# Optimization experiments

Hardware: AMD Instinct MI355X
Metric: run time of the kernel (lower is better)

## Reference

```python
import jax, jax.numpy as jnp
import numpy as np

B, C, D, H = 128, 8, 1024, 8
K_RANGE = (2, 3, 4, 5)


def setup_inputs() -> dict:
    key = jax.random.key(0)
    ks = jax.random.split(key, 10)
    s = 0.02
    return {
        "x": jax.random.normal(ks[0], (B, D), jnp.float32),
        # per-K prototype groups, shape (nb_classes, K, embed_dim) as in get_prototype_group()
        "p2": jax.random.normal(ks[1], (C, 2, D), jnp.float32),
        "p3": jax.random.normal(ks[2], (C, 3, D), jnp.float32),
        "p4": jax.random.normal(ks[3], (C, 4, D), jnp.float32),
        "p5": jax.random.normal(ks[4], (C, 5, D), jnp.float32),
        # per-class attention Block params (stacked over class axis)
        "ln_g": jnp.ones((C, D), jnp.float32),
        "ln_b": jnp.zeros((C, D), jnp.float32),
        "w_qkv": jax.random.normal(ks[5], (C, 3 * D, D), jnp.float32) * s,
        "b_qkv": jnp.zeros((C, 3 * D), jnp.float32),
        "w_proj": jax.random.normal(ks[6], (C, D, D), jnp.float32) * s,
        "b_proj": jnp.zeros((C, D), jnp.float32),
        # cls head
        "w_cls": jax.random.normal(ks[7], (C, D), jnp.float32) * s,
        "b_cls": jnp.zeros((C,), jnp.float32),
    }


def _proto_group(x, pg):
    """x: (B,D); pg: (C,K,D). Returns nearest proto (B,D), per-sample class group (B,K,D), class ids (B,)."""
    Cc, K, d = pg.shape
    flat = pg.reshape(Cc * K, d)
    # squared L2 distances (argmin identical to torch.cdist p=2 argmin)
    d2 = (jnp.sum(x * x, axis=1, keepdims=True)
          - 2.0 * (x @ flat.T)
          + jnp.sum(flat * flat, axis=1))
    idx = jnp.argmin(d2, axis=1)          # (B,)
    cls = idx // K                        # (B,)
    return flat[idx], pg[cls], cls


def _vicreg(x, nearest, proto_space, sim_c=25.0, std_c=25.0, cov_c=1.0):
    # sim: pull x toward its nearest prototype in every K-group
    repr_loss = jnp.mean((x[:, None, :] - nearest) ** 2)
    # std over batch of prototype space, unbiased var, eps=1e-4
    std = jnp.sqrt(jnp.var(proto_space, axis=0, ddof=1) + 1e-4)   # (S,D)
    std_loss = jnp.mean(jax.nn.relu(1.0 - std))
    # covariance of centered flattened prototype space
    ps = proto_space - jnp.mean(proto_space, axis=0)
    P = ps.reshape(-1, ps.shape[-1])                              # (B*S, D)
    cov = P.T @ P / (P.shape[0] - 1)
    cov_loss = ((cov ** 2).sum() - (jnp.diagonal(cov) ** 2).sum()) / ps.shape[-1]
    return sim_c * repr_loss + std_c * std_loss + cov_c * cov_loss


def _forward(x, p2, p3, p4, p5, ln_g, ln_b, w_qkv, b_qkv, w_proj, b_proj, w_cls, b_cls):
    groups = (p2, p3, p4, p5)
    nearest_list, space_list, cls = [], [], None
    for pg in groups:
        n, sp, cls = _proto_group(x, pg)   # cls kept from LAST group, as in torch code
        nearest_list.append(n)
        space_list.append(sp)
    nearest = jnp.stack(nearest_list, axis=1)     # (B, len(K_range), D)
    proto_space = jnp.concatenate(space_list, 1)  # (B, sum(K_range), D)

    vcr = _vicreg(x, nearest, proto_space)

    # per-class attention Block: LayerNorm -> MHA -> residual, vectorized over class axis c
    S = proto_space.shape[1]
    mu = proto_space.mean(-1, keepdims=True)
    var = proto_space.var(-1, keepdims=True)
    xn = (proto_space - mu) * jax.lax.rsqrt(var + 1e-5)               # (B,S,D)
    h = xn[None] * ln_g[:, None, None, :] + ln_b[:, None, None, :]    # (C,B,S,D)

    qkv = jnp.einsum('cbsd,cfd->cbsf', h, w_qkv) + b_qkv[:, None, None, :]
    dh = D // H
    qkv = qkv.reshape(C, B, S, 3, H, dh).transpose(3, 0, 1, 4, 2, 5)  # (3,C,B,H,S,dh)
    q, k, v = qkv[0] * (dh ** -0.5), qkv[1], qkv[2]
    attn = jax.nn.softmax(jnp.einsum('cbhqe,cbhke->cbhqk', q, k), axis=-1)
    o = jnp.einsum('cbhqk,cbhke->cbhqe', attn, v)                     # (C,B,H,S,dh)
    o = o.transpose(0, 1, 3, 2, 4).reshape(C, B, S, D)
    out = jnp.einsum('cbsd,ced->cbse', o, w_proj) + b_proj[:, None, None, :]
    attended = proto_space[None] + out                                # (C,B,S,D)

    # route each sample through the block of its (last-group) assigned class
    cond = attended[cls, jnp.arange(B)]                               # (B,S,D)
    cond = cond / jnp.maximum(jnp.linalg.norm(cond, axis=2, keepdims=True), 1e-12)
    pooled = cond.mean(1)                                             # (B,D)
    logits = pooled @ w_cls.T + b_cls
    return logits, vcr


def reference(x, p2, p3, p4, p5, ln_g, ln_b, w_qkv, b_qkv, w_proj, b_proj, w_cls, b_cls):
    return _forward(x, p2, p3, p4, p5, ln_g, ln_b, w_qkv, b_qkv, w_proj, b_proj, w_cls, b_cls)
```

## Files before the change

### kernel.cpp

```cpp
#include <hip/hip_runtime.h>
#include <math.h>

#define NB 128
#define ND 1024
#define NS 14
#define NDH 128

typedef float f32x4 __attribute__((ext_vector_type(4)));
typedef short bf16x8 __attribute__((ext_vector_type(8)));
typedef unsigned int u32x4 __attribute__((ext_vector_type(4)));

__device__ __forceinline__ unsigned short f2bf(float v) {
  unsigned int u = __builtin_bit_cast(unsigned int, v);
  return (unsigned short)((u + 0x7FFFu + ((u >> 16) & 1u)) >> 16);
}
__device__ __forceinline__ float bf2f(unsigned short u) {
  return __builtin_bit_cast(float, (unsigned int)u << 16);
}

__device__ __forceinline__ bf16x8 pack_bv(float4 w0, float4 w1) {
  unsigned int u0, u1, u2, u3;
  asm("v_cvt_pk_bf16_f32 %0, %1, %2" : "=v"(u0) : "v"(w0.x), "v"(w0.y));
  asm("v_cvt_pk_bf16_f32 %0, %1, %2" : "=v"(u1) : "v"(w0.z), "v"(w0.w));
  asm("v_cvt_pk_bf16_f32 %0, %1, %2" : "=v"(u2) : "v"(w1.x), "v"(w1.y));
  asm("v_cvt_pk_bf16_f32 %0, %1, %2" : "=v"(u3) : "v"(w1.z), "v"(w1.w));
  u32x4 u = {u0, u1, u2, u3};
  return __builtin_bit_cast(bf16x8, u);
}

__device__ __forceinline__ void s_decomp(int s, int& g, int& k) {
  if (s < 2)      { g = 0; k = s; }
  else if (s < 5) { g = 1; k = s - 2; }
  else if (s < 9) { g = 2; k = s - 5; }
  else            { g = 3; k = s - 9; }
}
__device__ __forceinline__ const float* grp_ptr(int g, const float* p2, const float* p3,
                                                const float* p4, const float* p5) {
  return g == 0 ? p2 : g == 1 ? p3 : g == 2 ? p4 : p5;
}
__device__ __forceinline__ int grp_base(int g) { return g == 0 ? 0 : g == 1 ? 16 : g == 2 ? 40 : 72; }
__device__ __forceinline__ int grp_k(int g) { return g + 2; }

__global__ __launch_bounds__(256) void k_ln(
    const float* __restrict__ p2, const float* __restrict__ p3,
    const float* __restrict__ p4, const float* __restrict__ p5,
    const float* __restrict__ ln_g, const float* __restrict__ ln_b,
    unsigned short* __restrict__ hbf2, float* __restrict__ pall)
{
  int r = blockIdx.x, t = threadIdx.x;
  __shared__ __align__(16) float xs[ND];
  float4* xs4 = (float4*)xs;
  const float* pp; int idx;
  if (r < 16)      { pp = p2; idx = r; }
  else if (r < 40) { pp = p3; idx = r - 16; }
  else if (r < 72) { pp = p4; idx = r - 40; }
  else             { pp = p5; idx = r - 72; }
  const float4* row4 = (const float4*)(pp + (size_t)idx * ND);
  float4 v = row4[t];
  xs4[t] = v;
  float s1 = v.x + v.y + v.z + v.w;
  float s2 = v.x * v.x + v.y * v.y + v.z * v.z + v.w * v.w;
  __shared__ float ra[256], rb[256];
  ra[t] = s1; rb[t] = s2; __syncthreads();
  for (int o = 128; o > 0; o >>= 1) { if (t < o) { ra[t] += ra[t + o]; rb[t] += rb[t + o]; } __syncthreads(); }
  __shared__ float mu, rstd;
  if (t == 0) {
    float m = ra[0] * (1.f / 1024.f);
    float var = rb[0] * (1.f / 1024.f) - m * m;
    mu = m; rstd = rsqrtf(var + 1e-5f);
  }
  __syncthreads();
  ((float4*)(pall + (size_t)r * ND))[t] = xs4[t];
  float4 xv = xs4[t];
  float nx = (xv.x - mu) * rstd, ny = (xv.y - mu) * rstd,
        nz = (xv.z - mu) * rstd, nw = (xv.w - mu) * rstd;
  int d0 = t * 4;
  int m = r >> 4, rr = r & 15;
  int kblk = d0 >> 5, qq = (d0 >> 3) & 3, e0 = d0 & 7;
  size_t fidx = (size_t)kblk * 3584 + m * 512 + (qq * 16 + rr) * 8 + e0;
#pragma unroll
  for (int c = 0; c < 8; ++c) {
    float4 g = ((const float4*)(ln_g + (size_t)c * ND))[t];
    float4 bb = ((const float4*)(ln_b + (size_t)c * ND))[t];
    ushort4 u;
    u.x = f2bf(nx * g.x + bb.x); u.y = f2bf(ny * g.y + bb.y);
    u.z = f2bf(nz * g.z + bb.z); u.w = f2bf(nw * g.w + bb.w);
    *(ushort4*)&hbf2[(size_t)c * 114688 + fidx] = u;
  }
}

__global__ __launch_bounds__(512) void k_qkv_assign(
    const unsigned short* __restrict__ hbf2, const float* __restrict__ w_qkv,
    const float* __restrict__ b_qkv, unsigned short* __restrict__ qkv_bf,
    const float* __restrict__ x,
    const float* __restrict__ p2, const float* __restrict__ p3,
    const float* __restrict__ p4, const float* __restrict__ p5,
    int* __restrict__ cls, int* __restrict__ rows_g, float* __restrict__ minv)
{
  __shared__ __align__(16) float lred[3 * 2 * 7 * 256];
  int bid = blockIdx.x, t = threadIdx.x;
  if (bid < 768) {
    int c = bid / 96, xb = bid - c * 96;
    int lane = t & 63, wid = t >> 6;
    int cg = wid & 1, ks = wid >> 1;
    int r16 = lane & 15, q = lane >> 4;
    int col = xb * 32 + cg * 16 + r16;
    const float* Wp = w_qkv + ((size_t)c * 3072 + col) * ND + ks * 256 + q * 8;
    const unsigned short* Hp = hbf2 + (size_t)c * 114688 + (size_t)(ks * 8) * 3584 + lane * 8;
    f32x4 acc[7] = {};
#pragma unroll
    for (int i = 0; i < 8; ++i) {
      float4 w0 = *(const float4*)(Wp + i * 32);
      float4 w1 = *(const float4*)(Wp + i * 32 + 4);
      bf16x8 bv = pack_bv(w0, w1);
      const unsigned short* hk = Hp + (size_t)i * 3584;
#pragma unroll
      for (int m = 0; m < 7; ++m) {
        bf16x8 av = *(const bf16x8*)(hk + m * 512);
        acc[m] = __builtin_amdgcn_mfma_f32_16x16x32_bf16(av, bv, acc[m], 0, 0, 0);
      }
    }
    if (ks) {
#pragma unroll
      for (int m = 0; m < 7; ++m)
        *(f32x4*)&lred[(((ks - 1) * 2 + cg) * 7 + m) * 256 + lane * 4] = acc[m];
    }
    __syncthreads();
    if (ks == 0) {
      float bq = b_qkv[(size_t)c * 3072 + col];
#pragma unroll
      for (int m = 0; m < 7; ++m) {
        f32x4 a1 = *(const f32x4*)&lred[((0 * 2 + cg) * 7 + m) * 256 + lane * 4];
        f32x4 a2 = *(const f32x4*)&lred[((1 * 2 + cg) * 7 + m) * 256 + lane * 4];
        f32x4 a3 = *(const f32x4*)&lred[((2 * 2 + cg) * 7 + m) * 256 + lane * 4];
#pragma unroll
        for (int r = 0; r < 4; ++r) {
          int row = m * 16 + q * 4 + r;
          qkv_bf[((size_t)c * 112 + row) * 3072 + col] = f2bf(acc[m][r] + a1[r] + a2[r] + a3[r] + bq);
        }
      }
    }
  } else {
    int b = bid - 768;
    float4* xs4 = (float4*)lred;
    float* d2s = lred + 1024;
    int* cls_s = (int*)(lred + 1152);
    if (t < 256) {
      const float4* xg4 = (const float4*)(x + (size_t)b * ND);
      xs4[t] = xg4[t];
    }
    __syncthreads();
    if (t < 112) {
      const float* pp; int idx;
      if (t < 16)      { pp = p2; idx = t; }
      else if (t < 40) { pp = p3; idx = t - 16; }
      else if (t < 72) { pp = p4; idx = t - 40; }
      else             { pp = p5; idx = t - 72; }
      const float4* pr4 = (const float4*)(pp + (size_t)idx * ND);
      float acc = 0.f;
#pragma unroll 8
      for (int d = 0; d < 256; ++d) {
        float4 a = xs4[d], p = pr4[d];
        float dx = a.x - p.x, dy = a.y - p.y, dz = a.z - p.z, dw = a.w - p.w;
        acc += dx * dx + dy * dy + dz * dz + dw * dw;
      }
      d2s[t] = acc;
    }
    __syncthreads();
    if (t < 4) {
      int base = grp_base(t), kg = grp_k(t), cnt = 8 * kg;
      float mv = d2s[base]; int mi = 0;
      for (int j = 1; j < cnt; ++j) { float v = d2s[base + j]; if (v < mv) { mv = v; mi = j; } }
      int c = mi / kg;
      cls[b * 4 + t] = c; cls_s[t] = c;
      minv[b * 4 + t] = mv;
    }
    __syncthreads();
    if (t < NS) {
      int g, k; s_decomp(t, g, k);
      rows_g[b * NS + t] = grp_base(g) + cls_s[g] * grp_k(g) + k;
    }
  }
}

__global__ __launch_bounds__(128) void k_prep(
    const int* __restrict__ cls, const float* __restrict__ minv,
    int* __restrict__ counts, int* __restrict__ ccnt, int* __restrict__ order,
    int* __restrict__ posof, int* __restrict__ chunkidx, int* __restrict__ chunk_c,
    int* __restrict__ chunk_lo, int* __restrict__ chunkN, float* __restrict__ scal)
{
  __shared__ int cnt_s[32];
  __shared__ int cc_s[8];
  __shared__ float red[128];
  int t = threadIdx.x;
  if (t < 32) cnt_s[t] = 0;
  if (t < 8) cc_s[t] = 0;
  if (t < 4) scal[t] = 0.f;
  __syncthreads();
  int c3;
#pragma unroll
  for (int g = 0; g < 4; ++g) {
    int c = cls[t * 4 + g];
    atomicAdd(&cnt_s[g * 8 + c], 1);
    if (g == 3) c3 = c;
  }
  int pos = atomicAdd(&cc_s[c3], 1);
  order[c3 * 128 + pos] = t;
  posof[t] = pos;
  red[t] = minv[t * 4 + 0] + minv[t * 4 + 1] + minv[t * 4 + 2] + minv[t * 4 + 3];
  __syncthreads();
  for (int o = 64; o > 0; o >>= 1) { if (t < o) red[t] += red[t + o]; __syncthreads(); }
  if (t == 0) {
    scal[0] = red[0];
    int T = 0;
    for (int c = 0; c < 8; ++c) {
      chunkidx[c] = T;
      int nch = (cc_s[c] + 15) >> 4;
      for (int j = 0; j < nch; ++j) { chunk_c[T] = c; chunk_lo[T] = j * 16; ++T; }
    }
    chunkN[0] = T;
  }
  if (t < 32) counts[t] = cnt_s[t];
  if (t < 8) ccnt[t] = cc_s[t];
}

__global__ __launch_bounds__(256) void k_attn_stats(
    const unsigned short* __restrict__ qkv_bf, const int* __restrict__ cls,
    const int* __restrict__ rows_g, const int* __restrict__ posof,
    const int* __restrict__ chunkidx, unsigned short* __restrict__ obf2,
    const float* __restrict__ p2, const float* __restrict__ p3,
    const float* __restrict__ p4, const float* __restrict__ p5,
    const int* __restrict__ counts, float* __restrict__ M, float* __restrict__ scal)
{
  int bid = blockIdx.x, t = threadIdx.x;
  if (bid < 1024) {
    __shared__ __align__(16) float qs[NS * NDH], ks2[NS * NDH], vs[NS * NDH];
    __shared__ float sc[NS * NS];
    __shared__ int rg[NS];
    int h = bid & 7, b = bid >> 3;
    if (t < NS) rg[t] = rows_g[b * NS + t];
    __syncthreads();
    int cp = cls[b * 4 + 3];
    int pos = posof[b];
    size_t gbase = (size_t)(chunkidx[cp] + (pos >> 4)) * 229376;
    int slot = pos & 15;
    const float scale = 0.08838834764831843f;
    for (int i = t; i < NS * 32; i += 256) {
      int s = i >> 5, e4 = (i & 31) * 4;
      size_t base = ((size_t)cp * 112 + rg[s]) * 3072 + h * NDH + e4;
      ushort4 uq = *(const ushort4*)&qkv_bf[base];
      ushort4 uk = *(const ushort4*)&qkv_bf[base + 1024];
      ushort4 uv = *(const ushort4*)&qkv_bf[base + 2048];
      int o = s * NDH + e4;
      qs[o]     = bf2f(uq.x) * scale; qs[o + 1] = bf2f(uq.y) * scale;
      qs[o + 2] = bf2f(uq.z) * scale; qs[o + 3] = bf2f(uq.w) * scale;
      ks2[o]     = bf2f(uk.x); ks2[o + 1] = bf2f(uk.y);
      ks2[o + 2] = bf2f(uk.z); ks2[o + 3] = bf2f(uk.w);
      vs[o]     = bf2f(uv.x); vs[o + 1] = bf2f(uv.y);
      vs[o + 2] = bf2f(uv.z); vs[o + 3] = bf2f(uv.w);
    }
    __syncthreads();
    if (t < NS * NS) {
      int si = t / NS, sj = t - (t / NS) * NS;
      const float4* qa = (const float4*)&qs[si * NDH];
      const float4* kb = (const float4*)&ks2[sj * NDH];
      float acc = 0.f;
#pragma unroll 8
      for (int e4 = 0; e4 < 32; ++e4) {
        float4 a = qa[e4], k4 = kb[e4];
        acc += a.x * k4.x + a.y * k4.y + a.z * k4.z + a.w * k4.w;
      }
      sc[t] = acc;
    }
    __syncthreads();
    if (t < NS) {
      float mx = -1e30f;
      for (int j = 0; j < NS; ++j) mx = fmaxf(mx, sc[t * NS + j]);
      float e_[NS]; float sum = 0.f;
      for (int j = 0; j < NS; ++j) { float e = expf(sc[t * NS + j] - mx); e_[j] = e; sum += e; }
      float inv = 1.f / sum;
      for (int j = 0; j < NS; ++j) sc[t * NS + j] = e_[j] * inv;
    }
    __syncthreads();
    for (int i = t; i < NS * 32; i += 256) {
      int s = i >> 5, e4 = i & 31;
      float4 a = {0.f, 0.f, 0.f, 0.f};
#pragma unroll
      for (int j = 0; j < NS; ++j) {
        float w = sc[s * NS + j];
        float4 v4 = ((const float4*)&vs[j * NDH])[e4];
        a.x += w * v4.x; a.y += w * v4.y; a.z += w * v4.z; a.w += w * v4.w;
      }
      int row = slot * 14 + s;
      int m = row >> 4, r16 = row & 15;
      int d0 = h * NDH + e4 * 4;
      int kblk = d0 >> 5, qq = (d0 >> 3) & 3, e0 = d0 & 7;
      ushort4 u; u.x = f2bf(a.x); u.y = f2bf(a.y); u.z = f2bf(a.z); u.w = f2bf(a.w);
      *(ushort4*)&obf2[gbase + (size_t)kblk * 7168 + m * 512 + (qq * 16 + r16) * 8 + e0] = u;
    }
  } else {
    int idx = (bid - 1024) * 256 + t;
    int s = idx >> 10, d = idx & 1023;
    int g, k; s_decomp(s, g, k);
    const float* pp = grp_ptr(g, p2, p3, p4, p5);
    int kg = grp_k(g);
    float vc[8], nc[8];
    float sum = 0.f, sumsq = 0.f;
#pragma unroll
    for (int c = 0; c < 8; ++c) {
      float v = pp[((size_t)(c * kg + k)) * ND + d];
      float n = (float)counts[g * 8 + c];
      vc[c] = v; nc[c] = n;
      sum += n * v; sumsq += n * v * v;
    }
    float mean = sum * (1.f / 128.f);
    float var = (sumsq - 128.f * mean * mean) * (1.f / 127.f);
    float sd = sqrtf(var + 1e-4f);
#pragma unroll
    for (int c = 0; c < 8; ++c)
      M[((size_t)(s * 8 + c)) * ND + d] = sqrtf(nc[c] * (1.f / 1791.f)) * (vc[c] - mean);
    float part = fmaxf(1.f - sd, 0.f);
    __shared__ float red[256];
    red[t] = part; __syncthreads();
    for (int o = 128; o > 0; o >>= 1) { if (t < o) red[t] += red[t + o]; __syncthreads(); }
    if (t == 0) atomicAdd(&scal[1], red[0]);
  }
}

__global__ __launch_bounds__(512) void k_proj_gram(
    const unsigned short* __restrict__ obf2, const int* __restrict__ order,
    const int* __restrict__ ccnt, const int* __restrict__ chunk_c,
    const int* __restrict__ chunk_lo, const int* __restrict__ chunkN,
    const int* __restrict__ rows_g,
    const float* __restrict__ w_proj, const float* __restrict__ b_proj,
    const float* __restrict__ pall, float* __restrict__ att,
    const float* __restrict__ M, float* __restrict__ scal)
{
  int bid = blockIdx.x, t = threadIdx.x;
  if (bid < 960) {
    int g = bid / 64, xb = bid - g * 64;
    if (g >= chunkN[0]) return;
    __shared__ __align__(16) float lred[3 * 2 * 7 * 256];
    __shared__ int sid_s[16];
    int c = chunk_c[g], lo = chunk_lo[g];
    int cnt = ccnt[c];
    int nb = cnt - lo; if (nb > 16) nb = 16;
    int lane = t & 63, wid = t >> 6;
    int rh = wid & 1, ks = wid >> 1;
    if (t < 16) sid_s[t] = order[c * 128 + lo + ((t < nb) ? t : nb - 1)];
    int r16 = lane & 15, q = lane >> 4;
    int col = xb * 16 + r16;
    const float* Wp = w_proj + ((size_t)c * ND + col) * ND + ks * 256 + q * 8;
    const unsigned short* Ap = obf2 + (size_t)g * 229376 + (size_t)(ks * 8) * 7168 + rh * 3584 + lane * 8;
    f32x4 acc[7] = {};
#pragma unroll
    for (int i = 0; i < 8; ++i) {
      float4 w0 = *(const float4*)(Wp + i * 32);
      float4 w1 = *(const float4*)(Wp + i * 32 + 4);
      bf16x8 bv = pack_bv(w0, w1);
      const unsigned short* ak = Ap + (size_t)i * 7168;
#pragma unroll
      for (int m = 0; m < 7; ++m) {
        bf16x8 av = *(const bf16x8*)(ak + m * 512);
        acc[m] = __builtin_amdgcn_mfma_f32_16x16x32_bf16(av, bv, acc[m], 0, 0, 0);
      }
    }
    if (ks) {
#pragma unroll
      for (int m = 0; m < 7; ++m)
        *(f32x4*)&lred[(((ks - 1) * 2 + rh) * 7 + m) * 256 + lane * 4] = acc[m];
    }
    __syncthreads();
    if (ks == 0) {
      float bp = b_proj[(size_t)c * ND + col];
#pragma unroll
      for (int m = 0; m < 7; ++m) {
        f32x4 a1 = *(const f32x4*)&lred[((0 * 2 + rh) * 7 + m) * 256 + lane * 4];
        f32x4 a2 = *(const f32x4*)&lred[((1 * 2 + rh) * 7 + m) * 256 + lane * 4];
        f32x4 a3 = *(const f32x4*)&lred[((2 * 2 + rh) * 7 + m) * 256 + lane * 4];
#pragma unroll
        for (int r = 0; r < 4; ++r) {
          int row = rh * 112 + m * 16 + q * 4 + r;
          int slot = row / 14, s = row - slot * 14;
          if (slot < nb) {
            int b = sid_s[slot];
            float res = pall[(size_t)rows_g[b * NS + s] * ND + col];
            att[((size_t)b * NS + s) * ND + col] = acc[m][r] + a1[r] + a2[r] + a3[r] + bp + res;
          }
        }
      }
    }
  } else if (bid < 1072) {
    int r = bid - 960;
    __shared__ __align__(16) float mi[ND];
    __shared__ float red2[128];
    float4* mi4 = (float4*)mi;
    const float4* src4 = (const float4*)(M + (size_t)r * ND);
    if (t < 256) mi4[t] = src4[t];
    if (t < 128) red2[t] = 0.f;
    __syncthreads();
    int j = t >> 2, qd = t & 3;
    float p = 0.f;
    if (j < 112) {
      const float4* mj4 = (const float4*)(M + (size_t)j * ND);
      float acc = 0.f;
#pragma unroll 8
      for (int d = qd * 64; d < qd * 64 + 64; ++d) {
        float4 a = mi4[d], b = mj4[d];
        acc += a.x * b.x + a.y * b.y + a.z * b.z + a.w * b.w;
      }
      acc += __shfl_xor(acc, 1, 4);
      acc += __shfl_xor(acc, 2, 4);
      p = acc * acc;
    }
    if (qd == 0 && j < 112) red2[j] = p;
    __syncthreads();
    for (int o = 64; o > 0; o >>= 1) { if (t < o) red2[t] += red2[t + o]; __syncthreads(); }
    if (t == 0) atomicAdd(&scal[2], red2[0]);
  } else {
    int d = (bid - 1072) * 512 + t;
    float tsum = 0.f;
    for (int r = 0; r < 112; ++r) { float v = M[(size_t)r * ND + d]; tsum += v * v; }
    __shared__ float red3[512];
    red3[t] = tsum * tsum; __syncthreads();
    for (int o = 256; o > 0; o >>= 1) { if (t < o) red3[t] += red3[t + o]; __syncthreads(); }
    if (t == 0) atomicAdd(&scal[3], red3[0]);
  }
}

__global__ __launch_bounds__(256) void k_final(
    const float* __restrict__ att, const float* __restrict__ w_cls,
    const float* __restrict__ b_cls, const float* __restrict__ scal,
    float* __restrict__ out)
{
  int b = blockIdx.x, t = threadIdx.x;
  __shared__ __align__(16) float as[NS * ND];
  __shared__ float wred[NS][4];
  __shared__ float inv[NS];
  __shared__ __align__(16) float pooled[ND];
  int lane = t & 63, w = t >> 6;
#pragma unroll
  for (int s = 0; s < NS; ++s) {
    float4 v = ((const float4*)(att + ((size_t)b * NS + s) * ND))[t];
    ((float4*)&as[s * ND])[t] = v;
    float p = v.x * v.x + v.y * v.y + v.z * v.z + v.w * v.w;
#pragma unroll
    for (int o = 32; o > 0; o >>= 1) p += __shfl_xor(p, o, 64);
    if (lane == 0) wred[s][w] = p;
  }
  __syncthreads();
  if (t < NS) {
    float s2 = wred[t][0] + wred[t][1] + wred[t][2] + wred[t][3];
    inv[t] = 1.f / fmaxf(sqrtf(s2), 1e-12f);
  }
  __syncthreads();
  float4 pa = {0.f, 0.f, 0.f, 0.f};
#pragma unroll
  for (int s = 0; s < NS; ++s) {
    float iv = inv[s];
    float4 v = ((const float4*)&as[s * ND])[t];
    pa.x += iv * v.x; pa.y += iv * v.y; pa.z += iv * v.z; pa.w += iv * v.w;
  }
  const float k14 = 1.f / 14.f;
  pa.x *= k14; pa.y *= k14; pa.z *= k14; pa.w *= k14;
  ((float4*)pooled)[t] = pa;
  __syncthreads();
  int c = t >> 5, l = t & 31;
  float acc = 0.f;
#pragma unroll
  for (int k = 0; k < 8; ++k) {
    int i4 = l + k * 32;
    float4 p4 = ((const float4*)pooled)[i4];
    float4 wc = ((const float4*)(w_cls + (size_t)c * ND))[i4];
    acc += p4.x * wc.x + p4.y * wc.y + p4.z * wc.z + p4.w * wc.w;
  }
  for (int o = 16; o > 0; o >>= 1) acc += __shfl_down(acc, o, 32);
  if (l == 0) out[b * 8 + c] = acc + b_cls[c];
  if (b == 0 && t == 0) {
    float repr = scal[0] * (1.f / (128.f * 4.f * 1024.f));
    float stdl = scal[1] * (1.f / 14336.f);
    float covl = (scal[2] - scal[3]) * (1.f / 1024.f);
    out[1024] = 25.f * repr + 25.f * stdl + covl;
  }
}

extern "C" void kernel_launch(void* const* d_in, const int* in_sizes, int n_in,
                              void* d_out, int out_size, void* d_ws, size_t ws_size,
                              hipStream_t stream) {
  const float* x      = (const float*)d_in[0];
  const float* p2     = (const float*)d_in[1];
  const float* p3     = (const float*)d_in[2];
  const float* p4     = (const float*)d_in[3];
  const float* p5     = (const float*)d_in[4];
  const float* ln_g   = (const float*)d_in[5];
  const float* ln_b   = (const float*)d_in[6];
  const float* w_qkv  = (const float*)d_in[7];
  const float* b_qkv  = (const float*)d_in[8];
  const float* w_proj = (const float*)d_in[9];
  const float* b_proj = (const float*)d_in[10];
  const float* w_cls  = (const float*)d_in[11];
  const float* b_cls  = (const float*)d_in[12];
  float* out = (float*)d_out;
  char* ws = (char*)d_ws;

  float* scal      = (float*)(ws + 0);
  int*   counts    = (int*)(ws + 64);
  int*   ccnt      = (int*)(ws + 192);
  int*   cls       = (int*)(ws + 256);
  int*   rows_g    = (int*)(ws + 2304);
  int*   order     = (int*)(ws + 9472);
  float* minv      = (float*)(ws + 13568);
  int*   posof     = (int*)(ws + 15616);
  int*   chunkidx  = (int*)(ws + 16128);
  int*   chunk_c   = (int*)(ws + 16160);
  int*   chunk_lo  = (int*)(ws + 16224);
  int*   chunkN    = (int*)(ws + 16288);
  float* pall      = (float*)(ws + 16384);
  unsigned short* hbf2 = (unsigned short*)(ws + 475136);
  unsigned short* qkvb = (unsigned short*)(ws + 2310144);
  unsigned short* obf2 = (unsigned short*)(ws + 7815168);
  float* att       = (float*)(ws + 15155200);
  float* M         = (float*)(ws + 22495232);

  k_ln<<<112, 256, 0, stream>>>(p2, p3, p4, p5, ln_g, ln_b, hbf2, pall);
  k_qkv_assign<<<896, 512, 0, stream>>>(hbf2, w_qkv, b_qkv, qkvb,
                                        x, p2, p3, p4, p5, cls, rows_g, minv);
  k_prep<<<1, 128, 0, stream>>>(cls, minv, counts, ccnt, order, posof, chunkidx, chunk_c, chunk_lo, chunkN, scal);
  k_attn_stats<<<1080, 256, 0, stream>>>(qkvb, cls, rows_g, posof, chunkidx, obf2,
                                         p2, p3, p4, p5, counts, M, scal);
  k_proj_gram<<<1074, 512, 0, stream>>>(obf2, order, ccnt, chunk_c, chunk_lo, chunkN, rows_g,
                                        w_proj, b_proj, pall, att, M, scal);
  k_final<<<128, 256, 0, stream>>>(att, w_cls, b_cls, scal, out);
}
```

Baseline: 124.0 us.

## Regroup prologue kernels: fuse LN with assignment, QKV GEMM with prep

Moves the nearest-prototype assignment out of the QKV GEMM kernel and into the LayerNorm kernel, and folds the single-block prep kernel into the QKV GEMM launch as block 0. This cuts one kernel launch and its dependency gap. The QKV GEMM now uses 256-thread blocks where each wave computes two 16-column tiles and reuses the loaded activation fragments, which halves the activation loads per MFMA and sets an occupancy hint. The assignment distance loop is split across two threads per prototype with a shuffle reduction. The risk is higher register pressure in the GEMM from the doubled accumulators.

New measurement: 119.0 us. -4.0%, faster.

```diff
diff --git a/kernel.cpp b/kernel.cpp
--- a/kernel.cpp
+++ b/kernel.cpp
@@ -41,136 +41,87 @@
 __device__ __forceinline__ int grp_base(int g) { return g == 0 ? 0 : g == 1 ? 16 : g == 2 ? 40 : 72; }
 __device__ __forceinline__ int grp_k(int g) { return g + 2; }
 
-__global__ __launch_bounds__(256) void k_ln(
+__global__ __launch_bounds__(256) void k_ln_assign(
+    const float* __restrict__ x,
     const float* __restrict__ p2, const float* __restrict__ p3,
     const float* __restrict__ p4, const float* __restrict__ p5,
     const float* __restrict__ ln_g, const float* __restrict__ ln_b,
-    unsigned short* __restrict__ hbf2, float* __restrict__ pall)
+    unsigned short* __restrict__ hbf2, float* __restrict__ pall,
+    int* __restrict__ cls, int* __restrict__ rows_g, float* __restrict__ minv)
 {
-  int r = blockIdx.x, t = threadIdx.x;
+  int bid = blockIdx.x, t = threadIdx.x;
   __shared__ __align__(16) float xs[ND];
   float4* xs4 = (float4*)xs;
-  const float* pp; int idx;
-  if (r < 16)      { pp = p2; idx = r; }
-  else if (r < 40) { pp = p3; idx = r - 16; }
-  else if (r < 72) { pp = p4; idx = r - 40; }
-  else             { pp = p5; idx = r - 72; }
-  const float4* row4 = (const float4*)(pp + (size_t)idx * ND);
-  float4 v = row4[t];
-  xs4[t] = v;
-  float s1 = v.x + v.y + v.z + v.w;
-  float s2 = v.x * v.x + v.y * v.y + v.z * v.z + v.w * v.w;
-  __shared__ float ra[256], rb[256];
-  ra[t] = s1; rb[t] = s2; __syncthreads();
-  for (int o = 128; o > 0; o >>= 1) { if (t < o) { ra[t] += ra[t + o]; rb[t] += rb[t + o]; } __syncthreads(); }
-  __shared__ float mu, rstd;
-  if (t == 0) {
-    float m = ra[0] * (1.f / 1024.f);
-    float var = rb[0] * (1.f / 1024.f) - m * m;
-    mu = m; rstd = rsqrtf(var + 1e-5f);
-  }
-  __syncthreads();
-  ((float4*)(pall + (size_t)r * ND))[t] = xs4[t];
-  float4 xv = xs4[t];
-  float nx = (xv.x - mu) * rstd, ny = (xv.y - mu) * rstd,
-        nz = (xv.z - mu) * rstd, nw = (xv.w - mu) * rstd;
-  int d0 = t * 4;
-  int m = r >> 4, rr = r & 15;
-  int kblk = d0 >> 5, qq = (d0 >> 3) & 3, e0 = d0 & 7;
-  size_t fidx = (size_t)kblk * 3584 + m * 512 + (qq * 16 + rr) * 8 + e0;
-#pragma unroll
-  for (int c = 0; c < 8; ++c) {
-    float4 g = ((const float4*)(ln_g + (size_t)c * ND))[t];
-    float4 bb = ((const float4*)(ln_b + (size_t)c * ND))[t];
-    ushort4 u;
-    u.x = f2bf(nx * g.x + bb.x); u.y = f2bf(ny * g.y + bb.y);
-    u.z = f2bf(nz * g.z + bb.z); u.w = f2bf(nw * g.w + bb.w);
-    *(ushort4*)&hbf2[(size_t)c * 114688 + fidx] = u;
-  }
-}
-
-__global__ __launch_bounds__(512) void k_qkv_assign(
-    const unsigned short* __restrict__ hbf2, const float* __restrict__ w_qkv,
-    const float* __restrict__ b_qkv, unsigned short* __restrict__ qkv_bf,
-    const float* __restrict__ x,
-    const float* __restrict__ p2, const float* __restrict__ p3,
-    const float* __restrict__ p4, const float* __restrict__ p5,
-    int* __restrict__ cls, int* __restrict__ rows_g, float* __restrict__ minv)
-{
-  __shared__ __align__(16) float lred[3 * 2 * 7 * 256];
-  int bid = blockIdx.x, t = threadIdx.x;
-  if (bid < 768) {
-    int c = bid / 96, xb = bid - c * 96;
-    int lane = t & 63, wid = t >> 6;
-    int cg = wid & 1, ks = wid >> 1;
-    int r16 = lane & 15, q = lane >> 4;
-    int col = xb * 32 + cg * 16 + r16;
-    const float* Wp = w_qkv + ((size_t)c * 3072 + col) * ND + ks * 256 + q * 8;
-    const unsigned short* Hp = hbf2 + (size_t)c * 114688 + (size_t)(ks * 8) * 3584 + lane * 8;
-    f32x4 acc[7] = {};
-#pragma unroll
-    for (int i = 0; i < 8; ++i) {
-      float4 w0 = *(const float4*)(Wp + i * 32);
-      float4 w1 = *(const float4*)(Wp + i * 32 + 4);
-      bf16x8 bv = pack_bv(w0, w1);
-      const unsigned short* hk = Hp + (size_t)i * 3584;
-#pragma unroll
-      for (int m = 0; m < 7; ++m) {
-        bf16x8 av = *(const bf16x8*)(hk + m * 512);
-        acc[m] = __builtin_amdgcn_mfma_f32_16x16x32_bf16(av, bv, acc[m], 0, 0, 0);
-      }
-    }
-    if (ks) {
-#pragma unroll
-      for (int m = 0; m < 7; ++m)
-        *(f32x4*)&lred[(((ks - 1) * 2 + cg) * 7 + m) * 256 + lane * 4] = acc[m];
-    }
-    __syncthreads();
-    if (ks == 0) {
-      float bq = b_qkv[(size_t)c * 3072 + col];
-#pragma unroll
-      for (int m = 0; m < 7; ++m) {
-        f32x4 a1 = *(const f32x4*)&lred[((0 * 2 + cg) * 7 + m) * 256 + lane * 4];
-        f32x4 a2 = *(const f32x4*)&lred[((1 * 2 + cg) * 7 + m) * 256 + lane * 4];
-        f32x4 a3 = *(const f32x4*)&lred[((2 * 2 + cg) * 7 + m) * 256 + lane * 4];
-#pragma unroll
-        for (int r = 0; r < 4; ++r) {
-          int row = m * 16 + q * 4 + r;
-          qkv_bf[((size_t)c * 112 + row) * 3072 + col] = f2bf(acc[m][r] + a1[r] + a2[r] + a3[r] + bq);
-        }
-      }
+  if (bid < 112) {
+    int r = bid;
+    const float* pp; int idx;
+    if (r < 16)      { pp = p2; idx = r; }
+    else if (r < 40) { pp = p3; idx = r - 16; }
+    else if (r < 72) { pp = p4; idx = r - 40; }
+    else             { pp = p5; idx = r - 72; }
+    const float4* row4 = (const float4*)(pp + (size_t)idx * ND);
+    float4 v = row4[t];
+    xs4[t] = v;
+    float s1 = v.x + v.y + v.z + v.w;
+    float s2 = v.x * v.x + v.y * v.y + v.z * v.z + v.w * v.w;
+    __shared__ float ra[256], rb[256];
+    ra[t] = s1; rb[t] = s2; __syncthreads();
+    for (int o = 128; o > 0; o >>= 1) { if (t < o) { ra[t] += ra[t + o]; rb[t] += rb[t + o]; } __syncthreads(); }
+    __shared__ float mu, rstd;
+    if (t == 0) {
+      float m = ra[0] * (1.f / 1024.f);
+      float var = rb[0] * (1.f / 1024.f) - m * m;
+      mu = m; rstd = rsqrtf(var + 1e-5f);
+    }
+    __syncthreads();
+    ((float4*)(pall + (size_t)r * ND))[t] = xs4[t];
+    float4 xv = xs4[t];
+    float nx = (xv.x - mu) * rstd, ny = (xv.y - mu) * rstd,
+          nz = (xv.z - mu) * rstd, nw = (xv.w - mu) * rstd;
+    int d0 = t * 4;
+    int m = r >> 4, rr = r & 15;
+    int kblk = d0 >> 5, qq = (d0 >> 3) & 3, e0 = d0 & 7;
+    size_t fidx = (size_t)kblk * 3584 + m * 512 + (qq * 16 + rr) * 8 + e0;
+#pragma unroll
+    for (int c = 0; c < 8; ++c) {
+      float4 g = ((const float4*)(ln_g + (size_t)c * ND))[t];
+      float4 bb = ((const float4*)(ln_b + (size_t)c * ND))[t];
+      ushort4 u;
+      u.x = f2bf(nx * g.x + bb.x); u.y = f2bf(ny * g.y + bb.y);
+      u.z = f2bf(nz * g.z + bb.z); u.w = f2bf(nw * g.w + bb.w);
+      *(ushort4*)&hbf2[(size_t)c * 114688 + fidx] = u;
     }
   } else {
-    int b = bid - 768;
-    float4* xs4 = (float4*)lred;
-    float* d2s = lred + 1024;
-    int* cls_s = (int*)(lred + 1152);
-    if (t < 256) {
-      const float4* xg4 = (const float4*)(x + (size_t)b * ND);
-      xs4[t] = xg4[t];
-    }
-    __syncthreads();
-    if (t < 112) {
+    int b = bid - 112;
+    __shared__ float d2s[112];
+    __shared__ int cls_s[4];
+    const float4* xg4 = (const float4*)(x + (size_t)b * ND);
+    xs4[t] = xg4[t];
+    __syncthreads();
+    int j = t >> 1, half = t & 1;
+    if (j < 112) {
       const float* pp; int idx;
-      if (t < 16)      { pp = p2; idx = t; }
-      else if (t < 40) { pp = p3; idx = t - 16; }
-      else if (t < 72) { pp = p4; idx = t - 40; }
-      else             { pp = p5; idx = t - 72; }
+      if (j < 16)      { pp = p2; idx = j; }
+      else if (j < 40) { pp = p3; idx = j - 16; }
+      else if (j < 72) { pp = p4; idx = j - 40; }
+      else             { pp = p5; idx = j - 72; }
       const float4* pr4 = (const float4*)(pp + (size_t)idx * ND);
       float acc = 0.f;
+      int d0 = half * 128;
 #pragma unroll 8
-      for (int d = 0; d < 256; ++d) {
+      for (int d = d0; d < d0 + 128; ++d) {
         float4 a = xs4[d], p = pr4[d];
         float dx = a.x - p.x, dy = a.y - p.y, dz = a.z - p.z, dw = a.w - p.w;
         acc += dx * dx + dy * dy + dz * dz + dw * dw;
       }
-      d2s[t] = acc;
+      acc += __shfl_xor(acc, 1, 2);
+      if (half == 0) d2s[j] = acc;
     }
     __syncthreads();
     if (t < 4) {
       int base = grp_base(t), kg = grp_k(t), cnt = 8 * kg;
       float mv = d2s[base]; int mi = 0;
-      for (int j = 1; j < cnt; ++j) { float v = d2s[base + j]; if (v < mv) { mv = v; mi = j; } }
+      for (int jj = 1; jj < cnt; ++jj) { float v = d2s[base + jj]; if (v < mv) { mv = v; mi = jj; } }
       int c = mi / kg;
       cls[b * 4 + t] = c; cls_s[t] = c;
       minv[b * 4 + t] = mv;
@@ -183,45 +134,106 @@
   }
 }
 
-__global__ __launch_bounds__(128) void k_prep(
+__global__ __launch_bounds__(256, 4) void k_qkv_prep(
+    const unsigned short* __restrict__ hbf2, const float* __restrict__ w_qkv,
+    const float* __restrict__ b_qkv, unsigned short* __restrict__ qkv_bf,
     const int* __restrict__ cls, const float* __restrict__ minv,
     int* __restrict__ counts, int* __restrict__ ccnt, int* __restrict__ order,
     int* __restrict__ posof, int* __restrict__ chunkidx, int* __restrict__ chunk_c,
     int* __restrict__ chunk_lo, int* __restrict__ chunkN, float* __restrict__ scal)
 {
-  __shared__ int cnt_s[32];
-  __shared__ int cc_s[8];
-  __shared__ float red[128];
-  int t = threadIdx.x;
-  if (t < 32) cnt_s[t] = 0;
-  if (t < 8) cc_s[t] = 0;
-  if (t < 4) scal[t] = 0.f;
+  int bid = blockIdx.x, t = threadIdx.x;
+  if (bid == 0) {
+    __shared__ int cnt_s[32];
+    __shared__ int cc_s[8];
+    __shared__ float red[128];
+    if (t < 32) cnt_s[t] = 0;
+    if (t < 8) cc_s[t] = 0;
+    if (t < 4) scal[t] = 0.f;
+    __syncthreads();
+    if (t < 128) {
+      int c3;
+#pragma unroll
+      for (int g = 0; g < 4; ++g) {
+        int c = cls[t * 4 + g];
+        atomicAdd(&cnt_s[g * 8 + c], 1);
+        if (g == 3) c3 = c;
+      }
+      int pos = atomicAdd(&cc_s[c3], 1);
+      order[c3 * 128 + pos] = t;
+      posof[t] = pos;
+      red[t] = minv[t * 4 + 0] + minv[t * 4 + 1] + minv[t * 4 + 2] + minv[t * 4 + 3];
+    }
+    __syncthreads();
+    for (int o = 64; o > 0; o >>= 1) { if (t < o) red[t] += red[t + o]; __syncthreads(); }
+    if (t == 0) {
+      scal[0] = red[0];
+      int T = 0;
+      for (int c = 0; c < 8; ++c) {
+        chunkidx[c] = T;
+        int nch = (cc_s[c] + 15) >> 4;
+        for (int j = 0; j < nch; ++j) { chunk_c[T] = c; chunk_lo[T] = j * 16; ++T; }
+      }
+      chunkN[0] = T;
+    }
+    if (t < 32) counts[t] = cnt_s[t];
+    if (t < 8) ccnt[t] = cc_s[t];
+    return;
+  }
+  __shared__ __align__(16) float lred[3 * 14 * 256];
+  int qb = bid - 1;
+  int c = qb / 96, xb = qb - c * 96;
+  int lane = t & 63, ks = t >> 6;
+  int r16 = lane & 15, q = lane >> 4;
+  int col0 = xb * 32 + r16, col1 = col0 + 16;
+  const float* Wp0 = w_qkv + ((size_t)c * 3072 + col0) * ND + ks * 256 + q * 8;
+  const float* Wp1 = Wp0 + (size_t)16 * ND;
+  const unsigned short* Hp = hbf2 + (size_t)c * 114688 + (size_t)(ks * 8) * 3584 + lane * 8;
+  f32x4 acc0[7] = {}, acc1[7] = {};
+#pragma unroll
+  for (int i = 0; i < 8; ++i) {
+    float4 w00 = *(const float4*)(Wp0 + i * 32);
+    float4 w01 = *(const float4*)(Wp0 + i * 32 + 4);
+    float4 w10 = *(const float4*)(Wp1 + i * 32);
+    float4 w11 = *(const float4*)(Wp1 + i * 32 + 4);
+    bf16x8 av[7];
+#pragma unroll
+    for (int m = 0; m < 7; ++m) av[m] = *(const bf16x8*)(Hp + (size_t)i * 3584 + m * 512);
+    bf16x8 bv0 = pack_bv(w00, w01);
+    bf16x8 bv1 = pack_bv(w10, w11);
+#pragma unroll
+    for (int m = 0; m < 7; ++m) {
+      acc0[m] = __builtin_amdgcn_mfma_f32_16x16x32_bf16(av[m], bv0, acc0[m], 0, 0, 0);
+      acc1[m] = __builtin_amdgcn_mfma_f32_16x16x32_bf16(av[m], bv1, acc1[m], 0, 0, 0);
+    }
+  }
+  if (ks) {
+#pragma unroll
+    for (int m = 0; m < 7; ++m) {
+      *(f32x4*)&lred[((ks - 1) * 14 + m) * 256 + lane * 4] = acc0[m];
+      *(f32x4*)&lred[((ks - 1) * 14 + 7 + m) * 256 + lane * 4] = acc1[m];
+    }
+  }
   __syncthreads();
-  int c3;
-#pragma unroll
-  for (int g = 0; g < 4; ++g) {
-    int c = cls[t * 4 + g];
-    atomicAdd(&cnt_s[g * 8 + c], 1);
-    if (g == 3) c3 = c;
-  }
-  int pos = atomicAdd(&cc_s[c3], 1);
-  order[c3 * 128 + pos] = t;
-  posof[t] = pos;
-  red[t] = minv[t * 4 + 0] + minv[t * 4 + 1] + minv[t * 4 + 2] + minv[t * 4 + 3];
-  __syncthreads();
-  for (int o = 64; o > 0; o >>= 1) { if (t < o) red[t] += red[t + o]; __syncthreads(); }
-  if (t == 0) {
-    scal[0] = red[0];
-    int T = 0;
-    for (int c = 0; c < 8; ++c) {
-      chunkidx[c] = T;
-      int nch = (cc_s[c] + 15) >> 4;
-      for (int j = 0; j < nch; ++j) { chunk_c[T] = c; chunk_lo[T] = j * 16; ++T; }
-    }
-    chunkN[0] = T;
-  }
-  if (t < 32) counts[t] = cnt_s[t];
-  if (t < 8) ccnt[t] = cc_s[t];
+  if (ks == 0) {
+    float bq0 = b_qkv[(size_t)c * 3072 + col0];
+    float bq1 = b_qkv[(size_t)c * 3072 + col1];
+#pragma unroll
+    for (int m = 0; m < 7; ++m) {
+      f32x4 s0 = acc0[m], s1 = acc1[m];
+#pragma unroll
+      for (int sk = 0; sk < 3; ++sk) {
+        s0 += *(const f32x4*)&lred[(sk * 14 + m) * 256 + lane * 4];
+        s1 += *(const f32x4*)&lred[(sk * 14 + 7 + m) * 256 + lane * 4];
+      }
+#pragma unroll
+      for (int r = 0; r < 4; ++r) {
+        int row = m * 16 + q * 4 + r;
+        qkv_bf[((size_t)c * 112 + row) * 3072 + col0] = f2bf(s0[r] + bq0);
+        qkv_bf[((size_t)c * 112 + row) * 3072 + col1] = f2bf(s1[r] + bq1);
+      }
+    }
+  }
 }
 
 __global__ __launch_bounds__(256) void k_attn_stats(
@@ -522,10 +534,9 @@
   float* att       = (float*)(ws + 15155200);
   float* M         = (float*)(ws + 22495232);
 
-  k_ln<<<112, 256, 0, stream>>>(p2, p3, p4, p5, ln_g, ln_b, hbf2, pall);
-  k_qkv_assign<<<896, 512, 0, stream>>>(hbf2, w_qkv, b_qkv, qkvb,
-                                        x, p2, p3, p4, p5, cls, rows_g, minv);
-  k_prep<<<1, 128, 0, stream>>>(cls, minv, counts, ccnt, order, posof, chunkidx, chunk_c, chunk_lo, chunkN, scal);
+  k_ln_assign<<<240, 256, 0, stream>>>(x, p2, p3, p4, p5, ln_g, ln_b, hbf2, pall, cls, rows_g, minv);
+  k_qkv_prep<<<769, 256, 0, stream>>>(hbf2, w_qkv, b_qkv, qkvb, cls, minv,
+                                      counts, ccnt, order, posof, chunkidx, chunk_c, chunk_lo, chunkN, scal);
   k_attn_stats<<<1080, 256, 0, stream>>>(qkvb, cls, rows_g, posof, chunkidx, obf2,
                                          p2, p3, p4, p5, counts, M, scal);
   k_proj_gram<<<1074, 512, 0, stream>>>(obf2, order, ccnt, chunk_c, chunk_lo, chunkN, rows_g,
```
